# Kernel optimization log

Measured on AMD Instinct MI355X. Metric: run time of the kernel, lower is better.

Reference implementation:

```python
import jax, jax.numpy as jnp
import numpy as np

B, H, W, C = 16, 64, 64, 256
DIM = 256

def setup_inputs() -> dict:
    key = jax.random.key(0)
    ks = jax.random.split(key, 9)
    s_in = 1.0 / np.sqrt(C)
    x = jax.random.normal(ks[0], (B, H, W, C), dtype=jnp.float32)
    Wq = jax.random.normal(ks[1], (C, DIM), dtype=jnp.float32) * s_in
    bq = jnp.zeros((DIM,), dtype=jnp.float32)
    Wk = jax.random.normal(ks[2], (C, DIM), dtype=jnp.float32) * s_in
    bk = jnp.zeros((DIM,), dtype=jnp.float32)
    Wv = jax.random.normal(ks[3], (C, DIM), dtype=jnp.float32) * s_in
    bv = jnp.zeros((DIM,), dtype=jnp.float32)
    # 'out' conv sees 1 input channel (after the channel reduce_sum)
    Wo = jax.random.normal(ks[4], (1, DIM), dtype=jnp.float32)
    bo = jnp.zeros((DIM,), dtype=jnp.float32)
    return {"x": x, "Wq": Wq, "bq": bq, "Wk": Wk, "bk": bk,
            "Wv": Wv, "bv": bv, "Wo": Wo, "bo": bo}

def reference(x, Wq, bq, Wk, bk, Wv, bv, Wo, bo):
    # 1x1 convs == channel GEMMs
    q = jnp.einsum('bhwc,cd->bhwd', x, Wq) + bq
    k = jnp.einsum('bhwc,cd->bhwd', x, Wk) + bk
    v = jnp.einsum('bhwc,cd->bhwd', x, Wv) + bv
    # channel-reduce score -> [B,H,W,1], softmax jointly over spatial axes
    score = jnp.sum(q * k, axis=-1, keepdims=True)
    attn = jax.nn.softmax(score, axis=(1, 2))
    # channel-reduce of v weighted by per-pixel attn -> [B,H,W,1]
    out = jnp.sum(v * attn, axis=-1, keepdims=True)
    # final 1x1 conv: 1 input channel -> DIM output channels
    return jnp.einsum('bhwc,cd->bhwd', out, Wo) + bo
```

## Files before the change

kernel.cpp:

```cpp
#include <hip/hip_runtime.h>


typedef __bf16 bf16_t;
typedef __attribute__((ext_vector_type(8))) __bf16 bf16x8;
typedef __attribute__((ext_vector_type(4))) __bf16 bf16x4;
typedef __attribute__((ext_vector_type(4))) float f32x4;

#define NBATCH 16
#define NPIX   65536
#define PPB    4096

#define MH_OFF    0u
#define ML_OFF    131072u
#define U_OFF     262144u
#define WV_OFF    263168u
#define SCL_OFF   264192u
#define SCORE_OFF 264448u
#define SV_OFF    526592u
#define BMAX_OFF  788736u
#define BSUM_OFF  788800u

__global__ __launch_bounds__(256) void prep_kernel(
    const float* __restrict__ Wq, const float* __restrict__ bq,
    const float* __restrict__ Wk, const float* __restrict__ bk,
    const float* __restrict__ Wv, const float* __restrict__ bv,
    bf16_t* __restrict__ Mh, bf16_t* __restrict__ Ml,
    float* __restrict__ u, float* __restrict__ wv, float* __restrict__ scl)
{
    const int t = threadIdx.x;
    if (blockIdx.x < 256) {
        const int c = blockIdx.x;
        __shared__ __align__(16) float wq_row[256];
        wq_row[t] = Wq[c * 256 + t];
        __syncthreads();
        const float4* wk4 = (const float4*)(Wk + t * 256);
        const float4* wq4 = (const float4*)wq_row;
        float acc = 0.f;
#pragma unroll 8
        for (int i = 0; i < 64; ++i) {
            float4 a = wq4[i], b = wk4[i];
            acc += a.x * b.x + a.y * b.y + a.z * b.z + a.w * b.w;
        }
        bf16_t h = (bf16_t)acc;
        float hf = (float)h;
        bf16_t l = (bf16_t)(acc - hf);
        Mh[c * 256 + t] = h;
        Ml[c * 256 + t] = l;
    } else {
        float uacc = 0.f, wvacc = 0.f;
        const float* wqr = Wq + t * 256;
        const float* wkr = Wk + t * 256;
        const float* wvr = Wv + t * 256;
#pragma unroll 4
        for (int d = 0; d < 256; ++d) {
            uacc += wqr[d] * bk[d] + wkr[d] * bq[d];
            wvacc += wvr[d];
        }
        u[t] = uacc;
        wv[t] = wvacc;
        __shared__ float r1[256], r2[256];
        r1[t] = bq[t] * bk[t];
        r2[t] = bv[t];
        __syncthreads();
        for (int s = 128; s > 0; s >>= 1) {
            if (t < s) { r1[t] += r1[t + s]; r2[t] += r2[t + s]; }
            __syncthreads();
        }
        if (t == 0) { scl[0] = r1[0]; scl[1] = r2[0]; }
    }
}

__device__ __forceinline__ int swz(int row, int col) {
    return row * 256 + (col ^ ((row & 7) << 3));
}

__global__ __launch_bounds__(512, 4) void score_kernel(
    const float* __restrict__ x,
    const bf16_t* __restrict__ Mh, const bf16_t* __restrict__ Ml,
    const float* __restrict__ u, const float* __restrict__ wvp,
    const float* __restrict__ scl,
    float* __restrict__ score, float* __restrict__ svout)
{
    __shared__ __align__(16) char smem[65536];
    __shared__ float svp[64], tpp[64];
    bf16_t* Ah = (bf16_t*)smem;
    bf16_t* Al = Ah + 16384;
    float* redS = (float*)smem;

    const int t = threadIdx.x;
    const int lane = t & 63;
    const int wid = t >> 6;
    const int l15 = lane & 15;
    const int lg = lane >> 4;
    const int pix0 = blockIdx.x * 64;
    const int wcol0 = wid * 32;

    const int srow = t >> 3;
    const int sch = (t & 7) * 16;
    const float* xrow = x + (size_t)(pix0 + srow) * 256;

    float sv_acc = 0.f, tp_acc = 0.f;

#define CVT_WRITE_DOTS(XV, H)                                                 \
    {                                                                         \
        _Pragma("unroll")                                                     \
        for (int j = 0; j < 2; ++j) {                                         \
            bf16x8 hi, lo;                                                    \
            _Pragma("unroll")                                                 \
            for (int e = 0; e < 8; ++e) {                                     \
                float f = ((const float*)XV)[j * 8 + e];                      \
                bf16_t h = (bf16_t)f;                                         \
                hi[e] = h;                                                    \
                lo[e] = (bf16_t)(f - (float)h);                               \
            }                                                                 \
            int idx = swz(srow, (H) * 128 + sch + j * 8);                     \
            *(bf16x8*)&Ah[idx] = hi;                                          \
            *(bf16x8*)&Al[idx] = lo;                                          \
        }                                                                     \
        _Pragma("unroll")                                                     \
        for (int i = 0; i < 4; ++i) {                                         \
            float4 wvv = *(const float4*)(wvp + (H) * 128 + sch + i * 4);     \
            float4 uvv = *(const float4*)(u + (H) * 128 + sch + i * 4);       \
            sv_acc += XV[i].x * wvv.x + XV[i].y * wvv.y +                     \
                      XV[i].z * wvv.z + XV[i].w * wvv.w;                      \
            tp_acc += XV[i].x * uvv.x + XV[i].y * uvv.y +                     \
                      XV[i].z * uvv.z + XV[i].w * uvv.w;                      \
        }                                                                     \
    }

    f32x4 acc[4][2];
#pragma unroll
    for (int i = 0; i < 4; ++i)
#pragma unroll
        for (int j = 0; j < 2; ++j)
            acc[i][j] = (f32x4){0.f, 0.f, 0.f, 0.f};

#define MFMA_HALF(H)                                                          \
    _Pragma("unroll")                                                         \
    for (int ks = (H) * 4; ks < (H) * 4 + 4; ++ks) {                          \
        const int k0 = ks * 32;                                               \
        bf16x8 afh[4], afl[4];                                                \
        _Pragma("unroll")                                                     \
        for (int rf = 0; rf < 4; ++rf) {                                      \
            int idx = swz(rf * 16 + l15, k0 + lg * 8);                        \
            afh[rf] = *(const bf16x8*)&Ah[idx];                               \
            afl[rf] = *(const bf16x8*)&Al[idx];                               \
        }                                                                     \
        bf16x8 bfh[2], bfl[2];                                                \
        _Pragma("unroll")                                                     \
        for (int cf = 0; cf < 2; ++cf) {                                      \
            size_t bo = (size_t)(wcol0 + cf * 16 + l15) * 256 + k0 + lg * 8;  \
            bfh[cf] = *(const bf16x8*)(Mh + bo);                              \
            bfl[cf] = *(const bf16x8*)(Ml + bo);                              \
        }                                                                     \
        _Pragma("unroll")                                                     \
        for (int rf = 0; rf < 4; ++rf)                                        \
            _Pragma("unroll")                                                 \
            for (int cf = 0; cf < 2; ++cf) {                                  \
                acc[rf][cf] = __builtin_amdgcn_mfma_f32_16x16x32_bf16(        \
                    afh[rf], bfh[cf], acc[rf][cf], 0, 0, 0);                  \
                acc[rf][cf] = __builtin_amdgcn_mfma_f32_16x16x32_bf16(        \
                    afl[rf], bfh[cf], acc[rf][cf], 0, 0, 0);                  \
                acc[rf][cf] = __builtin_amdgcn_mfma_f32_16x16x32_bf16(        \
                    afh[rf], bfl[cf], acc[rf][cf], 0, 0, 0);                  \
            }                                                                 \
    }

    float4 xva[4];
#pragma unroll
    for (int i = 0; i < 4; ++i) xva[i] = *(const float4*)(xrow + sch + i * 4);
    CVT_WRITE_DOTS(xva, 0);

    float4 xvb[4];
#pragma unroll
    for (int i = 0; i < 4; ++i) xvb[i] = *(const float4*)(xrow + 128 + sch + i * 4);

    __syncthreads();
    MFMA_HALF(0);

    CVT_WRITE_DOTS(xvb, 1);
#pragma unroll
    for (int m = 1; m < 8; m <<= 1) {
        sv_acc += __shfl_xor(sv_acc, m, 64);
        tp_acc += __shfl_xor(tp_acc, m, 64);
    }
    if ((lane & 7) == 0) { svp[srow] = sv_acc; tpp[srow] = tp_acc; }

    __syncthreads();
    MFMA_HALF(1);

    float sacc[4][4];
#pragma unroll
    for (int rf = 0; rf < 4; ++rf) {
#pragma unroll
        for (int r = 0; r < 4; ++r) {
            int row = rf * 16 + lg * 4 + r;
            float s = 0.f;
#pragma unroll
            for (int cf = 0; cf < 2; ++cf) {
                int idx = swz(row, wcol0 + cf * 16 + l15);
                float xv = (float)Ah[idx] + (float)Al[idx];
                s += xv * acc[rf][cf][r];
            }
#pragma unroll
            for (int m = 1; m < 16; m <<= 1) s += __shfl_xor(s, m, 64);
            sacc[rf][r] = s;
        }
    }
    __syncthreads();
    if (l15 == 0) {
#pragma unroll
        for (int rf = 0; rf < 4; ++rf)
#pragma unroll
            for (int r = 0; r < 4; ++r)
                redS[wid * 64 + rf * 16 + lg * 4 + r] = sacc[rf][r];
    }
    __syncthreads();
    if (t < 64) {
        float s = tpp[t] + scl[0];
#pragma unroll
        for (int w = 0; w < 8; ++w) s += redS[w * 64 + t];
        score[pix0 + t] = s;
        svout[pix0 + t] = svp[t] + scl[1];
    }
#undef CVT_WRITE_DOTS
#undef MFMA_HALF
}

__global__ __launch_bounds__(256) void stats_kernel(
    const float* __restrict__ score,
    float* __restrict__ bmax, float* __restrict__ bsum)
{
    const int b = blockIdx.x, t = threadIdx.x;
    const int lane = t & 63, wid = t >> 6;
    const float4* s4 = (const float4*)(score + b * PPB);
    float4 v[4];
#pragma unroll
    for (int i = 0; i < 4; ++i) v[i] = s4[t + i * 256];
    float m = v[0].x;
#pragma unroll
    for (int i = 0; i < 4; ++i) {
        m = fmaxf(m, fmaxf(fmaxf(v[i].x, v[i].y), fmaxf(v[i].z, v[i].w)));
    }
    float sum = 0.f;
#pragma unroll
    for (int i = 0; i < 4; ++i) {
        sum += __expf(v[i].x - m) + __expf(v[i].y - m) +
               __expf(v[i].z - m) + __expf(v[i].w - m);
    }
#pragma unroll
    for (int k = 1; k < 64; k <<= 1) {
        float om = __shfl_xor(m, k, 64);
        float os = __shfl_xor(sum, k, 64);
        float nm = fmaxf(m, om);
        sum = sum * __expf(m - nm) + os * __expf(om - nm);
        m = nm;
    }
    __shared__ float sm[4], ss[4];
    if (lane == 0) { sm[wid] = m; ss[wid] = sum; }
    __syncthreads();
    if (t == 0) {
        float M = fmaxf(fmaxf(sm[0], sm[1]), fmaxf(sm[2], sm[3]));
        float S = ss[0] * __expf(sm[0] - M) + ss[1] * __expf(sm[1] - M) +
                  ss[2] * __expf(sm[2] - M) + ss[3] * __expf(sm[3] - M);
        bmax[b] = M; bsum[b] = S;
    }
}

__global__ __launch_bounds__(256) void out_kernel(
    const float* __restrict__ score, const float* __restrict__ sv,
    const float* __restrict__ bmax, const float* __restrict__ bsum,
    const float* __restrict__ Wo, const float* __restrict__ bo,
    float* __restrict__ out)
{
    const int total = NPIX * 64;
    const int stride = gridDim.x * blockDim.x;
    for (int idx = blockIdx.x * blockDim.x + threadIdx.x; idx < total; idx += stride) {
        int p = idx >> 6;
        int c4 = (idx & 63) << 2;
        int b = p >> 12;
        float g = __expf(score[p] - bmax[b]) / bsum[b] * sv[p];
        float4 w = *(const float4*)(Wo + c4);
        float4 bb = *(const float4*)(bo + c4);
        float4 o = { g * w.x + bb.x, g * w.y + bb.y, g * w.z + bb.z, g * w.w + bb.w };
        *(float4*)(out + (size_t)p * 256 + c4) = o;
    }
}

extern "C" void kernel_launch(void* const* d_in, const int* in_sizes, int n_in,
                              void* d_out, int out_size, void* d_ws, size_t ws_size,
                              hipStream_t stream) {
    const float* x  = (const float*)d_in[0];
    const float* Wq = (const float*)d_in[1];
    const float* bq = (const float*)d_in[2];
    const float* Wk = (const float*)d_in[3];
    const float* bk = (const float*)d_in[4];
    const float* Wv = (const float*)d_in[5];
    const float* bv = (const float*)d_in[6];
    const float* Wo = (const float*)d_in[7];
    const float* bo = (const float*)d_in[8];
    float* out = (float*)d_out;
    char* ws = (char*)d_ws;

    bf16_t* Mh = (bf16_t*)(ws + MH_OFF);
    bf16_t* Ml = (bf16_t*)(ws + ML_OFF);
    float* u   = (float*)(ws + U_OFF);
    float* wv  = (float*)(ws + WV_OFF);
    float* scl = (float*)(ws + SCL_OFF);
    float* score = (float*)(ws + SCORE_OFF);
    float* sv    = (float*)(ws + SV_OFF);
    float* bmax  = (float*)(ws + BMAX_OFF);
    float* bsum  = (float*)(ws + BSUM_OFF);

    prep_kernel<<<dim3(257), dim3(256), 0, stream>>>(Wq, bq, Wk, bk, Wv, bv, Mh, Ml, u, wv, scl);
    score_kernel<<<dim3(NPIX / 64), dim3(512), 0, stream>>>(x, Mh, Ml, u, wv, scl, score, sv);
    stats_kernel<<<dim3(NBATCH), dim3(256), 0, stream>>>(score, bmax, bsum);
    out_kernel<<<dim3(4096), dim3(256), 0, stream>>>(score, sv, bmax, bsum, Wo, bo, out);
}
```

Before: 103.2 us.

## Process two pixel tiles per block with B fragments held in registers

Each score_kernel block now handles 128 pixels as two 64-pixel tiles. The per-wave Mh/Ml B fragments are loaded once into registers and reused across both tiles, and the next tile's x is prefetched during the current tile's MFMA. The reduction buffer moves to its own shared array so it no longer aliases the A tiles. Launch bounds drop from 4 to 2 blocks per CU so the larger register footprint fits, at the cost of occupancy and half as many blocks in the grid.

```diff
diff --git a/kernel.cpp b/kernel.cpp
--- a/kernel.cpp
+++ b/kernel.cpp
@@ -3,7 +3,6 @@
 
 typedef __bf16 bf16_t;
 typedef __attribute__((ext_vector_type(8))) __bf16 bf16x8;
-typedef __attribute__((ext_vector_type(4))) __bf16 bf16x4;
 typedef __attribute__((ext_vector_type(4))) float f32x4;
 
 #define NBATCH 16
@@ -74,7 +73,7 @@
     return row * 256 + (col ^ ((row & 7) << 3));
 }
 
-__global__ __launch_bounds__(512, 4) void score_kernel(
+__global__ __launch_bounds__(512, 2) void score_kernel(
     const float* __restrict__ x,
     const bf16_t* __restrict__ Mh, const bf16_t* __restrict__ Ml,
     const float* __restrict__ u, const float* __restrict__ wvp,
@@ -82,24 +81,30 @@
     float* __restrict__ score, float* __restrict__ svout)
 {
     __shared__ __align__(16) char smem[65536];
+    __shared__ float redS[8][64];
     __shared__ float svp[64], tpp[64];
     bf16_t* Ah = (bf16_t*)smem;
     bf16_t* Al = Ah + 16384;
-    float* redS = (float*)smem;
 
     const int t = threadIdx.x;
     const int lane = t & 63;
     const int wid = t >> 6;
     const int l15 = lane & 15;
     const int lg = lane >> 4;
-    const int pix0 = blockIdx.x * 64;
     const int wcol0 = wid * 32;
 
     const int srow = t >> 3;
     const int sch = (t & 7) * 16;
-    const float* xrow = x + (size_t)(pix0 + srow) * 256;
-
-    float sv_acc = 0.f, tp_acc = 0.f;
+
+    bf16x8 Bh[8][2], Bl[8][2];
+#pragma unroll
+    for (int kk = 0; kk < 8; ++kk)
+#pragma unroll
+        for (int cf = 0; cf < 2; ++cf) {
+            size_t bo = (size_t)(wcol0 + cf * 16 + l15) * 256 + kk * 32 + lg * 8;
+            Bh[kk][cf] = *(const bf16x8*)(Mh + bo);
+            Bl[kk][cf] = *(const bf16x8*)(Ml + bo);
+        }
 
 #define CVT_WRITE_DOTS(XV, H)                                                 \
     {                                                                         \
@@ -128,17 +133,11 @@
         }                                                                     \
     }
 
-    f32x4 acc[4][2];
-#pragma unroll
-    for (int i = 0; i < 4; ++i)
-#pragma unroll
-        for (int j = 0; j < 2; ++j)
-            acc[i][j] = (f32x4){0.f, 0.f, 0.f, 0.f};
-
 #define MFMA_HALF(H)                                                          \
     _Pragma("unroll")                                                         \
-    for (int ks = (H) * 4; ks < (H) * 4 + 4; ++ks) {                          \
-        const int k0 = ks * 32;                                               \
+    for (int ks = 0; ks < 4; ++ks) {                                          \
+        const int kk = (H) * 4 + ks;                                          \
+        const int k0 = kk * 32;                                               \
         bf16x8 afh[4], afl[4];                                                \
         _Pragma("unroll")                                                     \
         for (int rf = 0; rf < 4; ++rf) {                                      \
@@ -146,82 +145,96 @@
             afh[rf] = *(const bf16x8*)&Ah[idx];                               \
             afl[rf] = *(const bf16x8*)&Al[idx];                               \
         }                                                                     \
-        bf16x8 bfh[2], bfl[2];                                                \
-        _Pragma("unroll")                                                     \
-        for (int cf = 0; cf < 2; ++cf) {                                      \
-            size_t bo = (size_t)(wcol0 + cf * 16 + l15) * 256 + k0 + lg * 8;  \
-            bfh[cf] = *(const bf16x8*)(Mh + bo);                              \
-            bfl[cf] = *(const bf16x8*)(Ml + bo);                              \
-        }                                                                     \
         _Pragma("unroll")                                                     \
         for (int rf = 0; rf < 4; ++rf)                                        \
             _Pragma("unroll")                                                 \
             for (int cf = 0; cf < 2; ++cf) {                                  \
                 acc[rf][cf] = __builtin_amdgcn_mfma_f32_16x16x32_bf16(        \
-                    afh[rf], bfh[cf], acc[rf][cf], 0, 0, 0);                  \
+                    afh[rf], Bh[kk][cf], acc[rf][cf], 0, 0, 0);               \
                 acc[rf][cf] = __builtin_amdgcn_mfma_f32_16x16x32_bf16(        \
-                    afl[rf], bfh[cf], acc[rf][cf], 0, 0, 0);                  \
+                    afl[rf], Bh[kk][cf], acc[rf][cf], 0, 0, 0);               \
                 acc[rf][cf] = __builtin_amdgcn_mfma_f32_16x16x32_bf16(        \
-                    afh[rf], bfl[cf], acc[rf][cf], 0, 0, 0);                  \
+                    afh[rf], Bl[kk][cf], acc[rf][cf], 0, 0, 0);               \
             }                                                                 \
     }
 
-    float4 xva[4];
-#pragma unroll
-    for (int i = 0; i < 4; ++i) xva[i] = *(const float4*)(xrow + sch + i * 4);
-    CVT_WRITE_DOTS(xva, 0);
-
-    float4 xvb[4];
-#pragma unroll
-    for (int i = 0; i < 4; ++i) xvb[i] = *(const float4*)(xrow + 128 + sch + i * 4);
-
-    __syncthreads();
-    MFMA_HALF(0);
-
-    CVT_WRITE_DOTS(xvb, 1);
-#pragma unroll
-    for (int m = 1; m < 8; m <<= 1) {
-        sv_acc += __shfl_xor(sv_acc, m, 64);
-        tp_acc += __shfl_xor(tp_acc, m, 64);
-    }
-    if ((lane & 7) == 0) { svp[srow] = sv_acc; tpp[srow] = tp_acc; }
-
-    __syncthreads();
-    MFMA_HALF(1);
-
-    float sacc[4][4];
-#pragma unroll
-    for (int rf = 0; rf < 4; ++rf) {
-#pragma unroll
-        for (int r = 0; r < 4; ++r) {
-            int row = rf * 16 + lg * 4 + r;
-            float s = 0.f;
-#pragma unroll
-            for (int cf = 0; cf < 2; ++cf) {
-                int idx = swz(row, wcol0 + cf * 16 + l15);
-                float xv = (float)Ah[idx] + (float)Al[idx];
-                s += xv * acc[rf][cf][r];
+    float4 xva[4], xvb[4];
+    {
+        const float* xrow = x + (size_t)((size_t)blockIdx.x * 128 + srow) * 256;
+#pragma unroll
+        for (int i = 0; i < 4; ++i) xva[i] = *(const float4*)(xrow + sch + i * 4);
+    }
+
+#pragma unroll 2
+    for (int tt = 0; tt < 2; ++tt) {
+        const int pix0 = (blockIdx.x * 2 + tt) * 64;
+        const float* xrow = x + (size_t)(pix0 + srow) * 256;
+        float sv_acc = 0.f, tp_acc = 0.f;
+
+        f32x4 acc[4][2];
+#pragma unroll
+        for (int i = 0; i < 4; ++i)
+#pragma unroll
+            for (int j = 0; j < 2; ++j)
+                acc[i][j] = (f32x4){0.f, 0.f, 0.f, 0.f};
+
+        CVT_WRITE_DOTS(xva, 0);
+#pragma unroll
+        for (int i = 0; i < 4; ++i) xvb[i] = *(const float4*)(xrow + 128 + sch + i * 4);
+
+        __syncthreads();
+        MFMA_HALF(0);
+
+        CVT_WRITE_DOTS(xvb, 1);
+        if (tt == 0) {
+            const float* xrow2 = x + (size_t)(pix0 + 64 + srow) * 256;
+#pragma unroll
+            for (int i = 0; i < 4; ++i) xva[i] = *(const float4*)(xrow2 + sch + i * 4);
+        }
+#pragma unroll
+        for (int m = 1; m < 8; m <<= 1) {
+            sv_acc += __shfl_xor(sv_acc, m, 64);
+            tp_acc += __shfl_xor(tp_acc, m, 64);
+        }
+        if ((lane & 7) == 0) { svp[srow] = sv_acc; tpp[srow] = tp_acc; }
+
+        __syncthreads();
+        MFMA_HALF(1);
+
+        float sacc[4][4];
+#pragma unroll
+        for (int rf = 0; rf < 4; ++rf) {
+#pragma unroll
+            for (int r = 0; r < 4; ++r) {
+                int row = rf * 16 + lg * 4 + r;
+                float s = 0.f;
+#pragma unroll
+                for (int cf = 0; cf < 2; ++cf) {
+                    int idx = swz(row, wcol0 + cf * 16 + l15);
+                    float xv = (float)Ah[idx] + (float)Al[idx];
+                    s += xv * acc[rf][cf][r];
+                }
+#pragma unroll
+                for (int m = 1; m < 16; m <<= 1) s += __shfl_xor(s, m, 64);
+                sacc[rf][r] = s;
             }
-#pragma unroll
-            for (int m = 1; m < 16; m <<= 1) s += __shfl_xor(s, m, 64);
-            sacc[rf][r] = s;
-        }
-    }
-    __syncthreads();
-    if (l15 == 0) {
-#pragma unroll
-        for (int rf = 0; rf < 4; ++rf)
-#pragma unroll
-            for (int r = 0; r < 4; ++r)
-                redS[wid * 64 + rf * 16 + lg * 4 + r] = sacc[rf][r];
-    }
-    __syncthreads();
-    if (t < 64) {
-        float s = tpp[t] + scl[0];
-#pragma unroll
-        for (int w = 0; w < 8; ++w) s += redS[w * 64 + t];
-        score[pix0 + t] = s;
-        svout[pix0 + t] = svp[t] + scl[1];
+        }
+        __syncthreads();
+        if (l15 == 0) {
+#pragma unroll
+            for (int rf = 0; rf < 4; ++rf)
+#pragma unroll
+                for (int r = 0; r < 4; ++r)
+                    redS[wid][rf * 16 + lg * 4 + r] = sacc[rf][r];
+        }
+        __syncthreads();
+        if (t < 64) {
+            float s = tpp[t] + scl[0];
+#pragma unroll
+            for (int w = 0; w < 8; ++w) s += redS[w][t];
+            score[pix0 + t] = s;
+            svout[pix0 + t] = svp[t] + scl[1];
+        }
     }
 #undef CVT_WRITE_DOTS
 #undef MFMA_HALF
@@ -313,7 +326,7 @@
     float* bsum  = (float*)(ws + BSUM_OFF);
 
     prep_kernel<<<dim3(257), dim3(256), 0, stream>>>(Wq, bq, Wk, bk, Wv, bv, Mh, Ml, u, wv, scl);
-    score_kernel<<<dim3(NPIX / 64), dim3(512), 0, stream>>>(x, Mh, Ml, u, wv, scl, score, sv);
+    score_kernel<<<dim3(NPIX / 128), dim3(512), 0, stream>>>(x, Mh, Ml, u, wv, scl, score, sv);
     stats_kernel<<<dim3(NBATCH), dim3(256), 0, stream>>>(score, bmax, bsum);
     out_kernel<<<dim3(4096), dim3(256), 0, stream>>>(score, sv, bmax, bsum, Wo, bo, out);
 }
```

After: 115.1 us. 11.5% more time.
